# Kernel optimization log

Hardware: AMD Instinct MI355X
Metric: run time of the kernel (lower is better)

The kernel has to match this reference:

```python
import jax, jax.numpy as jnp
import numpy as np
from jax import lax


def setup_inputs() -> dict:
    key = jax.random.key(0)
    I = jax.random.uniform(key, (32, 3, 512, 512), dtype=jnp.float32)
    return {"I": I, "k": 15}


def reference(I, k):
    # Channel-wise min -> dark channel (torch does this via -max_pool over transposed channel dim)
    dark = jnp.min(I, axis=1, keepdims=True)  # [B,1,H,W]
    p = k // 2
    # Spatial min-pool kxk, stride 1, pad k//2. torch max_pool2d pads with -inf,
    # so the min-pool equivalent pads with +inf: reduce_window with min and +inf init.
    eroded = lax.reduce_window(
        dark,
        jnp.inf,
        lax.min,
        window_dimensions=(1, 1, k, k),
        window_strides=(1, 1, 1, 1),
        padding=[(0, 0), (0, 0), (p, p), (p, p)],
    )
    return eroded
```

## Files before the change

kernel.cpp:

```cpp
#include <hip/hip_runtime.h>
#include <math.h>

#define BATCH  32
#define CH     3
#define H      512
#define W      512
#define KWIN   15
#define PAD    7
#define TH     16
#define NRR    (TH + KWIN - 1)
#define STRIP  112
#define NSTRIP 5
#define NWAVES (BATCH * (H / TH) * NSTRIP)

static __device__ __forceinline__ float2 min2(float2 a, float2 b) {
    float2 r;
    r.x = fminf(a.x, b.x);
    r.y = fminf(a.y, b.y);
    return r;
}

__global__ void dcp_fused7(const float* __restrict__ I, float* __restrict__ out) {
    const int wid = blockIdx.x * 4 + (threadIdx.x >> 6);
    const int L   = threadIdx.x & 63;
    const int s   = wid % NSTRIP;
    const int rb  = (wid / NSTRIP) % (H / TH);
    const int b   = wid / (NSTRIP * (H / TH));
    const int y0  = rb * TH;
    const int f   = s * STRIP - 8 + 2 * L;
    const int cl  = min(max(f, 0), W - 2);
    const bool cv = (f >= 0) && (f < W);
    const bool st = (L >= 4) && (L <= 59) && (f < W);

    const float* base = I + (size_t)b * CH * H * W + cl;
    float* outb = out + (size_t)b * H * W;

    auto seqrow = [](int q) { return q < KWIN ? KWIN + q : 29 - q; };

    auto loadrow = [&](int i, float2& A, float2& B, float2& C) {
        const int yc = min(max(y0 - PAD + i, 0), H - 1);
        const float* p = base + (size_t)yc * W;
        A = *(const float2*)(p);
        B = *(const float2*)(p + (size_t)H * W);
        C = *(const float2*)(p + (size_t)2 * H * W);
    };

    auto hcompute = [&](int i, float2 A, float2 B, float2 C) -> float2 {
        const int y = y0 - PAD + i;
        float2 d = min2(min2(A, B), C);
        const bool pad = (y < 0) || (y >= H) || !cv;
        d.x = pad ? INFINITY : d.x;
        d.y = pad ? INFINITY : d.y;
        const float pm = fminf(d.x, d.y);
        const float t2 = fminf(pm, __shfl_down(pm, 1));
        const float t4 = fminf(t2, __shfl_down(t2, 2));
        const float q7 = fminf(t4, __shfl_up(t4, 3));
        float2 wv;
        wv.x = fminf(q7, __shfl_up(d.y, 4));
        wv.y = fminf(q7, __shfl_down(d.x, 4));
        return wv;
    };

    float2 Ab[3], Bb[3], Cb[3];
    loadrow(seqrow(0), Ab[0], Bb[0], Cb[0]);
    loadrow(seqrow(1), Ab[1], Bb[1], Cb[1]);

    float2 P[KWIN];
    float2 U;
    #pragma unroll
    for (int q = 0; q < NRR; ++q) {
        if (q + 2 < NRR)
            loadrow(seqrow(q + 2), Ab[(q + 2) % 3], Bb[(q + 2) % 3], Cb[(q + 2) % 3]);
        const float2 h = hcompute(seqrow(q), Ab[q % 3], Bb[q % 3], Cb[q % 3]);

        if (q == 0) {
            P[0] = h;
        } else if (q < KWIN) {
            P[q] = min2(P[q - 1], h);
            if (q == KWIN - 1 && st)
                *(float2*)(outb + (size_t)(y0 + 15) * W + f) = P[KWIN - 1];
        } else if (q == KWIN) {
            U = h;
            if (st) *(float2*)(outb + (size_t)(y0 + 14) * W + f) = min2(U, P[13]);
        } else if (q < NRR - 1) {
            const int r = 29 - q;
            U = min2(U, h);
            if (st) *(float2*)(outb + (size_t)(y0 + r) * W + f) = min2(U, P[r - 1]);
        } else {
            U = min2(U, h);
            if (st) *(float2*)(outb + (size_t)y0 * W + f) = U;
        }
    }
}

extern "C" void kernel_launch(void* const* d_in, const int* in_sizes, int n_in,
                              void* d_out, int out_size, void* d_ws, size_t ws_size,
                              hipStream_t stream) {
    const float* I = (const float*)d_in[0];
    float* out = (float*)d_out;
    dcp_fused7<<<dim3(NWAVES / 4), dim3(256), 0, stream>>>(I, out);
}
```

Measured before the change: 161.9 us.

## Split channel-min into a separate pass and pool over a precomputed dark map

Unfuses the kernel into two launches. The first computes the per-pixel channel minimum with float4 loads into a workspace buffer. The second runs the separable 15x15 min-pool over that single-channel map with a deeper 4-row load prefetch. The intent is to avoid re-reading all three input channels for every overlapping row window (about 1.9x row redundancy), at the cost of an extra write and read of the dark map plus a second launch.

```diff
diff --git a/kernel.cpp b/kernel.cpp
--- a/kernel.cpp
+++ b/kernel.cpp
@@ -19,8 +19,35 @@
     r.y = fminf(a.y, b.y);
     return r;
 }
+static __device__ __forceinline__ float4 min4(float4 a, float4 b) {
+    float4 r;
+    r.x = fminf(a.x, b.x); r.y = fminf(a.y, b.y);
+    r.z = fminf(a.z, b.z); r.w = fminf(a.w, b.w);
+    return r;
+}
 
-__global__ void dcp_fused7(const float* __restrict__ I, float* __restrict__ out) {
+__global__ void dcp_cmin(const float* __restrict__ I, float4* __restrict__ dark) {
+    const int tid = blockIdx.x * 256 + threadIdx.x;
+    const int PL  = (H * W) / 4;
+
+    float4 a[4], bv[4], c[4];
+    int d[4];
+    #pragma unroll
+    for (int j = 0; j < 4; ++j) {
+        d[j] = (tid & 255) + ((tid >> 8) * 4 + j) * 256;
+        const int b  = d[j] >> 16;
+        const int wi = d[j] & (PL - 1);
+        const float4* p = (const float4*)I + (size_t)b * 3 * PL + wi;
+        a[j]  = p[0];
+        bv[j] = p[PL];
+        c[j]  = p[2 * PL];
+    }
+    #pragma unroll
+    for (int j = 0; j < 4; ++j)
+        dark[d[j]] = min4(min4(a[j], bv[j]), c[j]);
+}
+
+__global__ void dcp_pool(const float* __restrict__ dark, float* __restrict__ out) {
     const int wid = blockIdx.x * 4 + (threadIdx.x >> 6);
     const int L   = threadIdx.x & 63;
     const int s   = wid % NSTRIP;
@@ -32,22 +59,18 @@
     const bool cv = (f >= 0) && (f < W);
     const bool st = (L >= 4) && (L <= 59) && (f < W);
 
-    const float* base = I + (size_t)b * CH * H * W + cl;
+    const float* base = dark + (size_t)b * H * W + cl;
     float* outb = out + (size_t)b * H * W;
 
     auto seqrow = [](int q) { return q < KWIN ? KWIN + q : 29 - q; };
 
-    auto loadrow = [&](int i, float2& A, float2& B, float2& C) {
+    auto loadrow = [&](int i) -> float2 {
         const int yc = min(max(y0 - PAD + i, 0), H - 1);
-        const float* p = base + (size_t)yc * W;
-        A = *(const float2*)(p);
-        B = *(const float2*)(p + (size_t)H * W);
-        C = *(const float2*)(p + (size_t)2 * H * W);
+        return *(const float2*)(base + (size_t)yc * W);
     };
 
-    auto hcompute = [&](int i, float2 A, float2 B, float2 C) -> float2 {
+    auto hcompute = [&](int i, float2 d) -> float2 {
         const int y = y0 - PAD + i;
-        float2 d = min2(min2(A, B), C);
         const bool pad = (y < 0) || (y >= H) || !cv;
         d.x = pad ? INFINITY : d.x;
         d.y = pad ? INFINITY : d.y;
@@ -61,34 +84,36 @@
         return wv;
     };
 
-    float2 Ab[3], Bb[3], Cb[3];
-    loadrow(seqrow(0), Ab[0], Bb[0], Cb[0]);
-    loadrow(seqrow(1), Ab[1], Bb[1], Cb[1]);
+    float2 D[4];
+    #pragma unroll
+    for (int j = 0; j < 4; ++j) D[j] = loadrow(seqrow(j));
 
     float2 P[KWIN];
     float2 U;
     #pragma unroll
     for (int q = 0; q < NRR; ++q) {
-        if (q + 2 < NRR)
-            loadrow(seqrow(q + 2), Ab[(q + 2) % 3], Bb[(q + 2) % 3], Cb[(q + 2) % 3]);
-        const float2 h = hcompute(seqrow(q), Ab[q % 3], Bb[q % 3], Cb[q % 3]);
-
-        if (q == 0) {
-            P[0] = h;
-        } else if (q < KWIN) {
-            P[q] = min2(P[q - 1], h);
+        if (q + 4 < NRR) {
+            const float2 nxt = loadrow(seqrow(q + 4));
+            const float2 h = hcompute(seqrow(q), D[q & 3]);
+            D[q & 3] = nxt;
+            if (q == 0)            P[0] = h;
+            else if (q < KWIN)     P[q] = min2(P[q - 1], h);
+            else if (q == KWIN)    U = h;
+            else                   U = min2(U, h);
             if (q == KWIN - 1 && st)
                 *(float2*)(outb + (size_t)(y0 + 15) * W + f) = P[KWIN - 1];
-        } else if (q == KWIN) {
-            U = h;
-            if (st) *(float2*)(outb + (size_t)(y0 + 14) * W + f) = min2(U, P[13]);
-        } else if (q < NRR - 1) {
+            if (q >= KWIN && st)
+                *(float2*)(outb + (size_t)(y0 + (29 - q)) * W + f) = min2(U, P[28 - q]);
+        } else {
+            const float2 h = hcompute(seqrow(q), D[q & 3]);
+            U = min2(U, h);
             const int r = 29 - q;
-            U = min2(U, h);
-            if (st) *(float2*)(outb + (size_t)(y0 + r) * W + f) = min2(U, P[r - 1]);
-        } else {
-            U = min2(U, h);
-            if (st) *(float2*)(outb + (size_t)y0 * W + f) = U;
+            if (st) {
+                if (r > 0)
+                    *(float2*)(outb + (size_t)(y0 + r) * W + f) = min2(U, P[r - 1]);
+                else
+                    *(float2*)(outb + (size_t)y0 * W + f) = U;
+            }
         }
     }
 }
@@ -97,6 +122,9 @@
                               void* d_out, int out_size, void* d_ws, size_t ws_size,
                               hipStream_t stream) {
     const float* I = (const float*)d_in[0];
-    float* out = (float*)d_out;
-    dcp_fused7<<<dim3(NWAVES / 4), dim3(256), 0, stream>>>(I, out);
+    float* out  = (float*)d_out;
+    float* dark = (float*)d_ws;
+
+    dcp_cmin<<<dim3(2048), dim3(256), 0, stream>>>(I, (float4*)dark);
+    dcp_pool<<<dim3(NWAVES / 4), dim3(256), 0, stream>>>(dark, out);
 }
```

After: 168.8 us. 4.2% more time.
